# Performance work log

Measured on AMD Instinct MI355X. Metric: run time of the kernel, lower is better.

## Reference

```python
import jax, jax.numpy as jnp
import numpy as np

EPS = 1e-5

def layer_norm(x, g, b):
    mu = jnp.mean(x, axis=-1, keepdims=True)
    var = jnp.mean(jnp.square(x - mu), axis=-1, keepdims=True)
    return (x - mu) * jax.lax.rsqrt(var + EPS) * g + b

def setup_inputs() -> dict:
    key = jax.random.key(0)
    B, N, IN_D, S, D = 64, 4096, 256, 8, 256
    ks = jax.random.split(key, 20)
    scale = lambda fan_in: 1.0 / np.sqrt(fan_in)
    u = lambda k, shape, s: jax.random.uniform(k, shape, jnp.float32, -s, s)
    return {
        "inputs": jax.random.normal(ks[0], (B, N, IN_D), jnp.float32),
        "noise": jax.random.normal(ks[1], (B, S, D), jnp.float32),
        "slots_mu": jax.random.normal(ks[2], (1, S, D), jnp.float32),
        "slots_sigma": jnp.ones((1, S, D), jnp.float32) * 0.1,
        "Wq": u(ks[3], (D, D), scale(D)), "bq": u(ks[4], (D,), scale(D)),
        "Wk": u(ks[5], (D, IN_D), scale(IN_D)), "bk": u(ks[6], (D,), scale(IN_D)),
        "Wv": u(ks[7], (D, IN_D), scale(IN_D)), "bv": u(ks[8], (D,), scale(IN_D)),
        "W_ih": u(ks[9], (3 * D, D), scale(D)), "b_ih": u(ks[10], (3 * D,), scale(D)),
        "W_hh": u(ks[11], (3 * D, D), scale(D)), "b_hh": u(ks[12], (3 * D,), scale(D)),
        "W1": u(ks[13], (D, D), scale(D)), "b1": u(ks[14], (D,), scale(D)),
        "W2": u(ks[15], (D, D), scale(D)), "b2": u(ks[16], (D,), scale(D)),
        "ln_slots_g": jnp.ones((D,), jnp.float32), "ln_slots_b": jnp.zeros((D,), jnp.float32),
        "ln_mlp_g": jnp.ones((D,), jnp.float32), "ln_mlp_b": jnp.zeros((D,), jnp.float32),
    }

def gru_cell(x, h, W_ih, b_ih, W_hh, b_hh):
    # PyTorch GRUCell: gates ordered (reset, update, new)
    gi = x @ W_ih.T + b_ih  # [B*S, 3D]
    gh = h @ W_hh.T + b_hh
    i_r, i_z, i_n = jnp.split(gi, 3, axis=-1)
    h_r, h_z, h_n = jnp.split(gh, 3, axis=-1)
    r = jax.nn.sigmoid(i_r + h_r)
    z = jax.nn.sigmoid(i_z + h_z)
    n = jnp.tanh(i_n + r * h_n)
    return (1.0 - z) * n + z * h

def reference(inputs, noise, slots_mu, slots_sigma, Wq, bq, Wk, bk, Wv, bv,
              W_ih, b_ih, W_hh, b_hh, W1, b1, W2, b2,
              ln_slots_g, ln_slots_b, ln_mlp_g, ln_mlp_b):
    B, N, _ = inputs.shape
    _, S, D = noise.shape
    num_iterations = 3
    slots = slots_mu + slots_sigma * noise  # [B, S, D]
    # k, v are loop-invariant; hoist the big GEMMs out of the iteration loop
    k = jnp.einsum('bnd,ed->bne', inputs, Wk) + bk  # [B, N, D]
    v = jnp.einsum('bnd,ed->bne', inputs, Wv) + bv  # [B, N, D]
    inv_sqrt_d = 1.0 / np.sqrt(D)
    for _ in range(num_iterations):
        slots_prev = slots
        q = layer_norm(slots, ln_slots_g, ln_slots_b) @ Wq.T + bq  # [B, S, D]
        attn_logits = jnp.einsum('bsd,bnd->bsn', q, k) * inv_sqrt_d
        attn = jax.nn.softmax(attn_logits, axis=-1)  # softmax over inputs (dim=-1)
        updates = jnp.einsum('bsn,bnd->bsd', attn, v)  # [B, S, D]
        h_new = gru_cell(updates.reshape(-1, D), slots_prev.reshape(-1, D),
                         W_ih, b_ih, W_hh, b_hh).reshape(B, S, D)
        slots = slots_prev + h_new  # residual around GRU (as in source)
        hidden = jax.nn.relu(layer_norm(slots, ln_mlp_g, ln_mlp_b) @ W1.T + b1)
        slots = slots + (hidden @ W2.T + b2)
    return slots
```

## Files before the change

### kernel.cpp

```cpp
#include <hip/hip_runtime.h>


constexpr int Bn = 64;
constexpr int Nn = 4096;
constexpr int Dd = 256;
constexpr int Ss = 8;
constexpr int CH = 16;
constexpr float EPSF = 1e-5f;

#define DEV __device__ __forceinline__

using short8 = __attribute__((ext_vector_type(8))) short;
using f32x4 = __attribute__((ext_vector_type(4))) float;
union U8 { short8 s; uint4 u; };

DEV unsigned bfpack2(float lo, float hi) {
  unsigned ul = __float_as_uint(lo), uh = __float_as_uint(hi);
  ul = (ul + 0x7FFFu + ((ul >> 16) & 1u)) >> 16;
  uh = (uh + 0x7FFFu + ((uh >> 16) & 1u)) & 0xFFFF0000u;
  return ul | uh;
}
DEV unsigned short bf16r(float x) {
  unsigned u = __float_as_uint(x);
  u = (u + 0x7FFFu + ((u >> 16) & 1u)) >> 16;
  return (unsigned short)u;
}
DEV float rsum32(float v) {
  v += __shfl_xor(v, 1); v += __shfl_xor(v, 2); v += __shfl_xor(v, 4);
  v += __shfl_xor(v, 8); v += __shfl_xor(v, 16);
  return v;
}
DEV float sigm(float x) { return 1.f / (1.f + __expf(-x)); }

template <int NK>
DEV void load_af(short8* a, const unsigned short* base, int lda, int m16, int quad) {
  const unsigned short* p = base + m16 * lda + quad * 8;
#pragma unroll
  for (int kk = 0; kk < NK; ++kk) a[kk] = *(const short8*)(p + kk * 32);
}
template <int NK>
DEV f32x4 gemm_tile(const short8* a, const unsigned short* wr, float binit) {
  f32x4 acc = {binit, binit, binit, binit};
#pragma unroll
  for (int kk = 0; kk < NK; ++kk) {
    short8 b = *(const short8*)(wr + kk * 32);
    acc = __builtin_amdgcn_mfma_f32_16x16x32_bf16(a[kk], b, acc, 0, 0, 0);
  }
  return acc;
}

DEV void ln_row8(const float* x, const float* g, const float* b, int d0,
                 unsigned short* dst) {
  float s = x[0] + x[1] + x[2] + x[3] + x[4] + x[5] + x[6] + x[7];
  float mu = rsum32(s) * (1.f / 256.f);
  float q = 0.f;
#pragma unroll
  for (int j = 0; j < 8; ++j) { float d = x[j] - mu; q += d * d; }
  float rs = rsqrtf(rsum32(q) * (1.f / 256.f) + EPSF);
  float o[8];
#pragma unroll
  for (int j = 0; j < 8; ++j) o[j] = (x[j] - mu) * rs * g[d0 + j] + b[d0 + j];
  uint4 w;
  w.x = bfpack2(o[0], o[1]); w.y = bfpack2(o[2], o[3]);
  w.z = bfpack2(o[4], o[5]); w.w = bfpack2(o[6], o[7]);
  *(uint4*)dst = w;
}

__global__ __launch_bounds__(256) void k_wqk(const float* __restrict__ Wq,
                                             const float* __restrict__ Wk,
                                             const float* __restrict__ bq,
                                             unsigned short* __restrict__ Wqk_b,
                                             float* __restrict__ bqk) {
  int tid = threadIdx.x, c = blockIdx.x;
  if (c < 256) {
    float acc = 0.f;
    for (int e = 0; e < 256; ++e) acc += Wq[e * 256 + tid] * Wk[e * 256 + c];
    Wqk_b[c * 256 + tid] = bf16r(acc);
  } else {
    float acc = 0.f;
    for (int e = 0; e < 256; ++e) acc += bq[e] * Wk[e * 256 + tid];
    bqk[tid] = acc;
  }
}

__global__ __launch_bounds__(256) void k_conv(
    const float* __restrict__ Wv, const float* __restrict__ Wih,
    const float* __restrict__ Whh, const float* __restrict__ W1,
    const float* __restrict__ W2,
    const float* __restrict__ bih, const float* __restrict__ bhh,
    unsigned* Wv_b, unsigned* Wzr_b, unsigned* Win_b, unsigned* Whn_b,
    unsigned* W1_b, unsigned* W2_b, float* bzr) {
  if (blockIdx.x >= 1152) {
    int i = (blockIdx.x - 1152) * 256 + threadIdx.x;
    if (i < 512) bzr[i] = bih[i] + bhh[i];
    return;
  }
  int p = blockIdx.x * 256 + threadIdx.x;
  const float* src; unsigned* dst;
  if (p < 32768) { src = Wv + 2 * p; dst = Wv_b + p; }
  else if (p < 163840) {
    int q = p - 32768, row = q >> 8, col = (q & 255) * 2;
    src = (col < 256) ? (Wih + row * 256 + col) : (Whh + row * 256 + col - 256);
    dst = Wzr_b + q;
  }
  else if (p < 196608) { int q = p - 163840; src = Wih + 512 * 256 + 2 * q; dst = Win_b + q; }
  else if (p < 229376) { int q = p - 196608; src = Whh + 512 * 256 + 2 * q; dst = Whn_b + q; }
  else if (p < 262144) { int q = p - 229376; src = W1 + 2 * q; dst = W1_b + q; }
  else { int q = p - 262144; src = W2 + 2 * q; dst = W2_b + q; }
  dst[0] = bfpack2(src[0], src[1]);
}

__global__ __launch_bounds__(256) void k_xconv(const float* __restrict__ xin,
                                               unsigned* __restrict__ xbf) {
#pragma unroll
  for (int j = 0; j < 4; ++j) {
    int flat = blockIdx.x * 1024 + j * 256 + threadIdx.x;
    const float4* src = (const float4*)(xin + (size_t)flat * 8);
    float4 v0 = src[0], v1 = src[1];
    uint4 o;
    o.x = bfpack2(v0.x, v0.y); o.y = bfpack2(v0.z, v0.w);
    o.z = bfpack2(v1.x, v1.y); o.w = bfpack2(v1.z, v1.w);
    ((uint4*)xbf)[flat] = o;
  }
}

__global__ __launch_bounds__(512) void k_qk0(const float* __restrict__ noise,
                                             const float* __restrict__ s_mu,
                                             const float* __restrict__ s_sg,
                                             const float* __restrict__ gsl,
                                             const float* __restrict__ bsl,
                                             const unsigned short* __restrict__ Wqk_b,
                                             const float* __restrict__ bqk,
                                             float* __restrict__ slots,
                                             float* __restrict__ qk) {
  __shared__ __align__(16) unsigned short lnb[16 * 264];
  const int tid = threadIdx.x, bb = blockIdx.x;
  const int lane = tid & 63, wave = tid >> 6;
  const int m16 = lane & 15, quad = lane >> 4;
  const int row = tid >> 5, l32 = tid & 31, d0 = l32 * 8;
  {
    const int grow = bb * 16 + row;
    const int sidx = (grow & 7) * 256 + d0;
    const float* np = noise + (size_t)grow * 256 + d0;
    float4 n0 = *(const float4*)np, n1 = *(const float4*)(np + 4);
    float4 m0 = *(const float4*)(s_mu + sidx), m1 = *(const float4*)(s_mu + sidx + 4);
    float4 g0 = *(const float4*)(s_sg + sidx), g1 = *(const float4*)(s_sg + sidx + 4);
    float x[8] = {m0.x + g0.x * n0.x, m0.y + g0.y * n0.y,
                  m0.z + g0.z * n0.z, m0.w + g0.w * n0.w,
                  m1.x + g1.x * n1.x, m1.y + g1.y * n1.y,
                  m1.z + g1.z * n1.z, m1.w + g1.w * n1.w};
    float* sp_ = slots + (size_t)grow * 256 + d0;
    float4 o0, o1;
    o0.x = x[0]; o0.y = x[1]; o0.z = x[2]; o0.w = x[3];
    o1.x = x[4]; o1.y = x[5]; o1.z = x[6]; o1.w = x[7];
    *(float4*)sp_ = o0; *(float4*)(sp_ + 4) = o1;
    ln_row8(x, gsl, bsl, d0, lnb + row * 264 + d0);
  }
  __syncthreads();
  short8 a8[8];
  load_af<8>(a8, lnb, 264, m16, quad);
#pragma unroll
  for (int i = 0; i < 2; ++i) {
    int t = wave + 8 * i;
    f32x4 acc = gemm_tile<8>(a8, Wqk_b + (size_t)(t * 16 + m16) * 256 + quad * 8,
                             bqk[t * 16 + m16]);
#pragma unroll
    for (int r = 0; r < 4; ++r)
      qk[(size_t)(bb * 16 + quad * 4 + r) * 256 + t * 16 + m16] = acc[r] * 0.0625f;
  }
}

__global__ __launch_bounds__(256) void k_attn(const unsigned* __restrict__ xbf,
                                              const float* __restrict__ qk,
                                              float* __restrict__ pl,
                                              float* __restrict__ pu) {
  __shared__ __align__(16) unsigned xt[2][128 * 65];
  __shared__ __align__(16) unsigned pp[2][32 * 17];
  __shared__ __align__(16) float lred[4][16];
  const int tid = threadIdx.x;
  const int lane = tid & 63, wave = tid >> 6;
  const int m16 = lane & 15, quad = lane >> 4;
  const int c = blockIdx.x, b = blockIdx.y;
  const int pb = (b * CH + c) * 8;
  const unsigned psel = (m16 & 1) ? 0x07060302u : 0x05040100u;

  short8 aq[8];
  {
    const float* qrow = qk + (size_t)(b * 8 + (m16 & 7)) * 256 + quad * 8;
#pragma unroll
    for (int kk = 0; kk < 8; ++kk) {
      U8 f;
      float4 q0 = *(const float4*)(qrow + kk * 32);
      float4 q1 = *(const float4*)(qrow + kk * 32 + 4);
      f.u.x = bfpack2(q0.x, q0.y); f.u.y = bfpack2(q0.z, q0.w);
      f.u.z = bfpack2(q1.x, q1.y); f.u.w = bfpack2(q1.z, q1.w);
      if (m16 >= 8) { f.u.x = 0u; f.u.y = 0u; f.u.z = 0u; f.u.w = 0u; }
      aq[kk] = f.s;
    }
  }
  float lacc[4] = {0.f, 0.f, 0.f, 0.f};
  f32x4 acc[4];
#pragma unroll
  for (int t = 0; t < 4; ++t) acc[t] = (f32x4){0.f, 0.f, 0.f, 0.f};
  const int d0w = wave * 64;

  const size_t row0 = (size_t)b * Nn + (size_t)c * 256;
  const uint4* xb4 = (const uint4*)xbf;

  uint4 pr[8];
#pragma unroll
  for (int i = 0; i < 8; ++i) {
    int flat = i * 256 + tid, n = flat >> 5, od = flat & 31;
    pr[i] = xb4[(row0 + n) * 32 + od];
  }

  for (int ch = 0; ch < 4; ++ch) {
    const int p = ch & 1;
    unsigned* xtb = xt[p];
#pragma unroll
    for (int i = 0; i < 8; ++i) {
      int flat = i * 256 + tid, n = flat >> 5, od = flat & 31, rb = od * 4;
      xtb[(rb + 0) * 65 + n] = pr[i].x;
      xtb[(rb + 1) * 65 + n] = pr[i].y;
      xtb[(rb + 2) * 65 + n] = pr[i].z;
      xtb[(rb + 3) * 65 + n] = pr[i].w;
    }
    if (ch + 1 < 4) {
      const size_t nb = row0 + (size_t)(ch + 1) * 64;
#pragma unroll
      for (int i = 0; i < 8; ++i) {
        int flat = i * 256 + tid, n = flat >> 5, od = flat & 31;
        pr[i] = xb4[(nb + n) * 32 + od];
      }
    }
    {
      const int nt = wave;
      const size_t arow = row0 + (size_t)ch * 64 + nt * 16 + m16;
      f32x4 pacc = (f32x4){0.f, 0.f, 0.f, 0.f};
#pragma unroll
      for (int kk = 0; kk < 8; ++kk) {
        U8 bf;
        bf.u = xb4[arow * 32 + kk * 4 + quad];
        pacc = __builtin_amdgcn_mfma_f32_16x16x32_bf16(aq[kk], bf.s, pacc, 0, 0, 0);
      }
      const int xrow = nt * 16 + m16;
      unsigned short* pps = (unsigned short*)pp[p];
#pragma unroll
      for (int r = 0; r < 4; ++r) {
        float pv = __expf(pacc[r]);
        lacc[r] += pv;
        pps[((xrow >> 1) * 17 + quad * 4 + r) * 2 + (xrow & 1)] = bf16r(pv);
      }
    }
    __syncthreads();
    const unsigned* ppb = pp[p];
#pragma unroll
    for (int nh = 0; nh < 2; ++nh) {
      U8 bp;
      bp.u.x = ppb[(nh * 16 + quad * 4 + 0) * 17 + m16];
      bp.u.y = ppb[(nh * 16 + quad * 4 + 1) * 17 + m16];
      bp.u.z = ppb[(nh * 16 + quad * 4 + 2) * 17 + m16];
      bp.u.w = ppb[(nh * 16 + quad * 4 + 3) * 17 + m16];
#pragma unroll
      for (int t = 0; t < 4; ++t) {
        int d = d0w + t * 16 + m16;
        const unsigned* xr = xtb + (d >> 1) * 65 + nh * 32 + quad * 8;
        unsigned u0 = xr[0], u1 = xr[1], u2 = xr[2], u3 = xr[3];
        unsigned u4 = xr[4], u5 = xr[5], u6 = xr[6], u7 = xr[7];
        U8 af;
        af.u.x = __builtin_amdgcn_perm(u1, u0, psel);
        af.u.y = __builtin_amdgcn_perm(u3, u2, psel);
        af.u.z = __builtin_amdgcn_perm(u5, u4, psel);
        af.u.w = __builtin_amdgcn_perm(u7, u6, psel);
        acc[t] = __builtin_amdgcn_mfma_f32_16x16x32_bf16(af.s, bp.s, acc[t], 0, 0, 0);
      }
    }
  }
  if (m16 < 8) {
#pragma unroll
    for (int t = 0; t < 4; ++t)
#pragma unroll
      for (int r = 0; r < 4; ++r)
        pu[(size_t)(pb + m16) * 256 + d0w + t * 16 + quad * 4 + r] = acc[t][r];
  }
#pragma unroll
  for (int r = 0; r < 4; ++r) {
    float v = lacc[r];
    v += __shfl_xor(v, 1); v += __shfl_xor(v, 2);
    v += __shfl_xor(v, 4); v += __shfl_xor(v, 8);
    if (m16 == 0) lred[wave][quad * 4 + r] = v;
  }
  __syncthreads();
  if (tid < 8)
    pl[pb + tid] = lred[0][tid] + lred[1][tid] + lred[2][tid] + lred[3][tid];
}

__global__ __launch_bounds__(512) void k_upd(
    const float* __restrict__ pl, const float* __restrict__ pu,
    const unsigned short* __restrict__ Wv_b, const float* __restrict__ bv,
    const unsigned short* __restrict__ Wzr_b, const float* __restrict__ bzr,
    const unsigned short* __restrict__ Win_b, const float* __restrict__ bin,
    const unsigned short* __restrict__ Whn_b, const float* __restrict__ bhn,
    const unsigned short* __restrict__ W1_b, const float* __restrict__ b1,
    const unsigned short* __restrict__ W2_b, const float* __restrict__ b2,
    const float* __restrict__ gml, const float* __restrict__ bml,
    const float* __restrict__ gsl, const float* __restrict__ bsl,
    const unsigned short* __restrict__ Wqk_b, const float* __restrict__ bqk,
    float* __restrict__ slots, float* __restrict__ qk, float* __restrict__ dout) {
  __shared__ __align__(16) unsigned short cat[16 * 520];
  __shared__ __align__(16) float sp[16 * 260];
  __shared__ __align__(16) float s1[16 * 260];
  __shared__ __align__(16) unsigned short lnb[16 * 264];
  const int tid = threadIdx.x, bb = blockIdx.x;
  const int lane = tid & 63, wave = tid >> 6;
  const int m16 = lane & 15, quad = lane >> 4;
  const int row = tid >> 5, l32 = tid & 31, d0 = l32 * 8;
  const int bat = 2 * bb + (row >> 3), sl = row & 7;
  {
    float L = 0.f;
#pragma unroll
    for (int cc = 0; cc < 16; ++cc) L += pl[(bat * 16 + cc) * 8 + sl];
    float li = 1.f / L;
    float a[8] = {0.f, 0.f, 0.f, 0.f, 0.f, 0.f, 0.f, 0.f};
    for (int cc = 0; cc < 16; ++cc) {
      const float* pp_ = pu + ((size_t)(bat * 16 + cc) * 8 + sl) * 256 + d0;
      float4 v0 = *(const float4*)pp_, v1 = *(const float4*)(pp_ + 4);
      a[0] += v0.x; a[1] += v0.y; a[2] += v0.z; a[3] += v0.w;
      a[4] += v1.x; a[5] += v1.y; a[6] += v1.z; a[7] += v1.w;
    }
    uint4 o;
    o.x = bfpack2(a[0] * li, a[1] * li); o.y = bfpack2(a[2] * li, a[3] * li);
    o.z = bfpack2(a[4] * li, a[5] * li); o.w = bfpack2(a[6] * li, a[7] * li);
    *(uint4*)(cat + row * 520 + d0) = o;
    const float* sp_ = slots + (size_t)(bb * 16 + row) * 256 + d0;
    float4 h0 = *(const float4*)sp_, h1 = *(const float4*)(sp_ + 4);
    *(float4*)(sp + row * 260 + d0) = h0;
    *(float4*)(sp + row * 260 + d0 + 4) = h1;
    uint4 hb;
    hb.x = bfpack2(h0.x, h0.y); hb.y = bfpack2(h0.z, h0.w);
    hb.z = bfpack2(h1.x, h1.y); hb.w = bfpack2(h1.z, h1.w);
    *(uint4*)(cat + row * 520 + 256 + d0) = hb;
  }
  __syncthreads();
  short8 afr[16];
  load_af<8>(afr, cat, 520, m16, quad);
  f32x4 accv[2];
#pragma unroll
  for (int i = 0; i < 2; ++i) {
    int t = wave + 8 * i;
    accv[i] = gemm_tile<8>(afr, Wv_b + (size_t)(t * 16 + m16) * 256 + quad * 8,
                           bv[t * 16 + m16]);
  }
  __syncthreads();
#pragma unroll
  for (int i = 0; i < 2; ++i) {
    int t = wave + 8 * i;
#pragma unroll
    for (int r = 0; r < 4; ++r)
      cat[(quad * 4 + r) * 520 + t * 16 + m16] = bf16r(accv[i][r]);
  }
  __syncthreads();
  load_af<16>(afr, cat, 520, m16, quad);
  f32x4 rr[2], zz[2];
#pragma unroll
  for (int i = 0; i < 2; ++i) {
    int t = wave + 8 * i;
    f32x4 ar = gemm_tile<16>(afr, Wzr_b + (size_t)(t * 16 + m16) * 512 + quad * 8,
                             bzr[t * 16 + m16]);
    f32x4 az = gemm_tile<16>(afr, Wzr_b + (size_t)((t + 16) * 16 + m16) * 512 + quad * 8,
                             bzr[(t + 16) * 16 + m16]);
#pragma unroll
    for (int r = 0; r < 4; ++r) { rr[i][r] = sigm(ar[r]); zz[i][r] = sigm(az[r]); }
  }
#pragma unroll
  for (int i = 0; i < 2; ++i) {
    int t = wave + 8 * i, col = t * 16 + m16;
    f32x4 ain = gemm_tile<8>(afr, Win_b + (size_t)(t * 16 + m16) * 256 + quad * 8,
                             bin[col]);
    f32x4 ahn = gemm_tile<8>(afr + 8, Whn_b + (size_t)(t * 16 + m16) * 256 + quad * 8,
                             bhn[col]);
#pragma unroll
    for (int r = 0; r < 4; ++r) {
      int rw = quad * 4 + r;
      float nin = ain[r] + rr[i][r] * ahn[r];
      float nn = 1.f - 2.f / (__expf(2.f * nin) + 1.f);
      float hpc = sp[rw * 260 + col];
      s1[rw * 260 + col] = hpc + (1.f - zz[i][r]) * nn + zz[i][r] * hpc;
    }
  }
  __syncthreads();
  {
    const float* s1r = s1 + row * 260 + d0;
    float4 v0 = *(const float4*)s1r, v1 = *(const float4*)(s1r + 4);
    float x[8] = {v0.x, v0.y, v0.z, v0.w, v1.x, v1.y, v1.z, v1.w};
    ln_row8(x, gml, bml, d0, lnb + row * 264 + d0);
  }
  __syncthreads();
  load_af<8>(afr, lnb, 264, m16, quad);
#pragma unroll
  for (int i = 0; i < 2; ++i) {
    int t = wave + 8 * i;
    f32x4 acc = gemm_tile<8>(afr, W1_b + (size_t)(t * 16 + m16) * 256 + quad * 8,
                             b1[t * 16 + m16]);
#pragma unroll
    for (int r = 0; r < 4; ++r)
      cat[(quad * 4 + r) * 520 + t * 16 + m16] = bf16r(fmaxf(acc[r], 0.f));
  }
  __syncthreads();
  load_af<8>(afr, cat, 520, m16, quad);
#pragma unroll
  for (int i = 0; i < 2; ++i) {
    int t = wave + 8 * i;
    f32x4 acc = gemm_tile<8>(afr, W2_b + (size_t)(t * 16 + m16) * 256 + quad * 8,
                             b2[t * 16 + m16]);
#pragma unroll
    for (int r = 0; r < 4; ++r) {
      int rw = quad * 4 + r, col = t * 16 + m16;
      float v = acc[r] + s1[rw * 260 + col];
      size_t gi = (size_t)(bb * 16 + rw) * 256 + col;
      slots[gi] = v;
      if (dout) dout[gi] = v;
      sp[rw * 260 + col] = v;
    }
  }
  __syncthreads();
  {
    const float* spr = sp + row * 260 + d0;
    float4 v0 = *(const float4*)spr, v1 = *(const float4*)(spr + 4);
    float x[8] = {v0.x, v0.y, v0.z, v0.w, v1.x, v1.y, v1.z, v1.w};
    ln_row8(x, gsl, bsl, d0, lnb + row * 264 + d0);
  }
  __syncthreads();
  load_af<8>(afr, lnb, 264, m16, quad);
#pragma unroll
  for (int i = 0; i < 2; ++i) {
    int t = wave + 8 * i;
    f32x4 acc = gemm_tile<8>(afr, Wqk_b + (size_t)(t * 16 + m16) * 256 + quad * 8,
                             bqk[t * 16 + m16]);
#pragma unroll
    for (int r = 0; r < 4; ++r)
      qk[(size_t)(bb * 16 + quad * 4 + r) * 256 + t * 16 + m16] = acc[r] * 0.0625f;
  }
}

extern "C" void kernel_launch(void* const* d_in, const int* in_sizes, int n_in,
                              void* d_out, int out_size, void* d_ws, size_t ws_size,
                              hipStream_t stream) {
  const float* inputs = (const float*)d_in[0];
  const float* noise = (const float*)d_in[1];
  const float* s_mu = (const float*)d_in[2];
  const float* s_sg = (const float*)d_in[3];
  const float* Wq = (const float*)d_in[4];
  const float* bq = (const float*)d_in[5];
  const float* Wk = (const float*)d_in[6];
  const float* Wv = (const float*)d_in[8];
  const float* bv = (const float*)d_in[9];
  const float* Wih = (const float*)d_in[10];
  const float* bih = (const float*)d_in[11];
  const float* Whh = (const float*)d_in[12];
  const float* bhh = (const float*)d_in[13];
  const float* W1 = (const float*)d_in[14];
  const float* b1 = (const float*)d_in[15];
  const float* W2 = (const float*)d_in[16];
  const float* b2 = (const float*)d_in[17];
  const float* gsl = (const float*)d_in[18];
  const float* bsl = (const float*)d_in[19];
  const float* gml = (const float*)d_in[20];
  const float* bml = (const float*)d_in[21];
  float* out = (float*)d_out;

  char* wsb = (char*)d_ws;
  unsigned* xbf = (unsigned*)wsb;
  float* fp = (float*)(wsb + (size_t)Bn * Nn * Dd * 2);
  float* slots = fp; fp += Bn * Ss * Dd;
  float* qk = fp;    fp += Bn * Ss * Dd;
  float* bqk = fp;   fp += Dd;
  float* pl = fp;    fp += Bn * CH * Ss;
  float* pu = fp;    fp += Bn * CH * Ss * Dd;
  float* bzr = fp;   fp += 512;
  unsigned short* wb = (unsigned short*)fp;
  unsigned short* Wv_b = wb;  wb += 65536;
  unsigned short* Wzr_b = wb; wb += 262144;
  unsigned short* Win_b = wb; wb += 65536;
  unsigned short* Whn_b = wb; wb += 65536;
  unsigned short* W1_b = wb;  wb += 65536;
  unsigned short* W2_b = wb;  wb += 65536;
  unsigned short* Wqk_b = wb; wb += 65536;
  (void)in_sizes; (void)n_in; (void)out_size; (void)ws_size;

  k_xconv<<<dim3(8192), dim3(256), 0, stream>>>(inputs, xbf);
  k_wqk<<<dim3(257), dim3(256), 0, stream>>>(Wq, Wk, bq, Wqk_b, bqk);
  k_conv<<<dim3(1154), dim3(256), 0, stream>>>(
      Wv, Wih, Whh, W1, W2, bih, bhh, (unsigned*)Wv_b, (unsigned*)Wzr_b,
      (unsigned*)Win_b, (unsigned*)Whn_b, (unsigned*)W1_b, (unsigned*)W2_b, bzr);
  k_qk0<<<dim3(32), dim3(512), 0, stream>>>(noise, s_mu, s_sg, gsl, bsl, Wqk_b, bqk,
                                            slots, qk);
  for (int it = 0; it < 3; ++it) {
    k_attn<<<dim3(CH, Bn), dim3(256), 0, stream>>>(xbf, qk, pl, pu);
    k_upd<<<dim3(32), dim3(512), 0, stream>>>(
        pl, pu, Wv_b, bv, Wzr_b, bzr, Win_b, bih + 512, Whn_b, bhh + 512, W1_b, b1,
        W2_b, b2, gml, bml, gsl, bsl, Wqk_b, bqk, slots, qk, (it == 2) ? out : nullptr);
  }
}
```

Baseline: 699.1 us.

## Quantize inputs and attention probs to FP8 and use fp8 MFMA in attention

Converts the pre-converted input tensor from bf16 to FP8 E4M3 via a software quantizer, halving the bytes streamed by each of the three attention passes. The attention kernel now uses fp8 MFMA for both the logits and the probs-times-inputs products, staging row and transposed copies in shared memory instead of reading rows twice from global. The qk scaling moves into the exp, and the weight-prep kernels are merged into one launch with an 8-column register-blocked Wq·Wk product. FP8 rounding of inputs, queries and softmax numerators may lose accuracy against the fp32 reference.

Measured after the change: 678.1 us. -3.0%, faster.

```diff
diff --git a/kernel.cpp b/kernel.cpp
--- a/kernel.cpp
+++ b/kernel.cpp
@@ -13,6 +13,7 @@
 using short8 = __attribute__((ext_vector_type(8))) short;
 using f32x4 = __attribute__((ext_vector_type(4))) float;
 union U8 { short8 s; uint4 u; };
+union LL { unsigned u[2]; long long l; };
 
 DEV unsigned bfpack2(float lo, float hi) {
   unsigned ul = __float_as_uint(lo), uh = __float_as_uint(hi);
@@ -25,6 +26,22 @@
   u = (u + 0x7FFFu + ((u >> 16) & 1u)) >> 16;
   return (unsigned short)u;
 }
+DEV unsigned f8q(float x) {
+  unsigned u = __float_as_uint(x), s = (u >> 24) & 0x80u;
+  float a = __uint_as_float(u & 0x7FFFFFFFu);
+  if (a >= 448.f) return s | 0x7Eu;
+  if (a < 0.015625f) {
+    int m = (int)rintf(a * 512.f);
+    return s | (unsigned)m;
+  }
+  unsigned v = (u & 0x7FFFFFFFu) + 0x7FFFFu + ((u >> 20) & 1u);
+  unsigned E = (v >> 23) - 120u;
+  unsigned M = (v >> 20) & 7u;
+  if (E > 15u) return s | 0x7Eu;
+  unsigned r = (E << 3) | M;
+  if (r > 0x7Eu) r = 0x7Eu;
+  return s | r;
+}
 DEV float rsum32(float v) {
   v += __shfl_xor(v, 1); v += __shfl_xor(v, 2); v += __shfl_xor(v, 4);
   v += __shfl_xor(v, 8); v += __shfl_xor(v, 16);
@@ -66,61 +83,65 @@
   *(uint4*)dst = w;
 }
 
-__global__ __launch_bounds__(256) void k_wqk(const float* __restrict__ Wq,
-                                             const float* __restrict__ Wk,
-                                             const float* __restrict__ bq,
-                                             unsigned short* __restrict__ Wqk_b,
-                                             float* __restrict__ bqk) {
-  int tid = threadIdx.x, c = blockIdx.x;
-  if (c < 256) {
-    float acc = 0.f;
-    for (int e = 0; e < 256; ++e) acc += Wq[e * 256 + tid] * Wk[e * 256 + c];
-    Wqk_b[c * 256 + tid] = bf16r(acc);
-  } else {
+__global__ __launch_bounds__(256) void k_prep(
+    const float* __restrict__ Wq, const float* __restrict__ Wk,
+    const float* __restrict__ bq, unsigned short* __restrict__ Wqk_b,
+    float* __restrict__ bqk, const float* __restrict__ Wv,
+    const float* __restrict__ Wih, const float* __restrict__ Whh,
+    const float* __restrict__ W1, const float* __restrict__ W2,
+    const float* __restrict__ bih, const float* __restrict__ bhh,
+    unsigned* Wv_b, unsigned* Wzr_b, unsigned* Win_b, unsigned* Whn_b,
+    unsigned* W1_b, unsigned* W2_b, float* bzr) {
+  const int u = blockIdx.x, tid = threadIdx.x;
+  if (u < 32) {
+    const int c0 = u * 8;
+    float acc[8] = {0.f, 0.f, 0.f, 0.f, 0.f, 0.f, 0.f, 0.f};
+    for (int e = 0; e < 256; ++e) {
+      float wq = Wq[e * 256 + tid];
+      const float* wk = Wk + e * 256 + c0;
+#pragma unroll
+      for (int j = 0; j < 8; ++j) acc[j] += wq * wk[j];
+    }
+#pragma unroll
+    for (int j = 0; j < 8; ++j) Wqk_b[(c0 + j) * 256 + tid] = bf16r(acc[j]);
+  } else if (u == 32) {
     float acc = 0.f;
     for (int e = 0; e < 256; ++e) acc += bq[e] * Wk[e * 256 + tid];
     bqk[tid] = acc;
-  }
-}
-
-__global__ __launch_bounds__(256) void k_conv(
-    const float* __restrict__ Wv, const float* __restrict__ Wih,
-    const float* __restrict__ Whh, const float* __restrict__ W1,
-    const float* __restrict__ W2,
-    const float* __restrict__ bih, const float* __restrict__ bhh,
-    unsigned* Wv_b, unsigned* Wzr_b, unsigned* Win_b, unsigned* Whn_b,
-    unsigned* W1_b, unsigned* W2_b, float* bzr) {
-  if (blockIdx.x >= 1152) {
-    int i = (blockIdx.x - 1152) * 256 + threadIdx.x;
-    if (i < 512) bzr[i] = bih[i] + bhh[i];
-    return;
-  }
-  int p = blockIdx.x * 256 + threadIdx.x;
-  const float* src; unsigned* dst;
-  if (p < 32768) { src = Wv + 2 * p; dst = Wv_b + p; }
-  else if (p < 163840) {
-    int q = p - 32768, row = q >> 8, col = (q & 255) * 2;
-    src = (col < 256) ? (Wih + row * 256 + col) : (Whh + row * 256 + col - 256);
-    dst = Wzr_b + q;
-  }
-  else if (p < 196608) { int q = p - 163840; src = Wih + 512 * 256 + 2 * q; dst = Win_b + q; }
-  else if (p < 229376) { int q = p - 196608; src = Whh + 512 * 256 + 2 * q; dst = Whn_b + q; }
-  else if (p < 262144) { int q = p - 229376; src = W1 + 2 * q; dst = W1_b + q; }
-  else { int q = p - 262144; src = W2 + 2 * q; dst = W2_b + q; }
-  dst[0] = bfpack2(src[0], src[1]);
+  } else {
+    int cu = u - 33;
+    if (cu >= 1152) {
+      int i = (cu - 1152) * 256 + tid;
+      if (i < 512) bzr[i] = bih[i] + bhh[i];
+      return;
+    }
+    int p = cu * 256 + tid;
+    const float* src; unsigned* dst;
+    if (p < 32768) { src = Wv + 2 * p; dst = Wv_b + p; }
+    else if (p < 163840) {
+      int q = p - 32768, row = q >> 8, col = (q & 255) * 2;
+      src = (col < 256) ? (Wih + row * 256 + col) : (Whh + row * 256 + col - 256);
+      dst = Wzr_b + q;
+    }
+    else if (p < 196608) { int q = p - 163840; src = Wih + 512 * 256 + 2 * q; dst = Win_b + q; }
+    else if (p < 229376) { int q = p - 196608; src = Whh + 512 * 256 + 2 * q; dst = Whn_b + q; }
+    else if (p < 262144) { int q = p - 229376; src = W1 + 2 * q; dst = W1_b + q; }
+    else { int q = p - 262144; src = W2 + 2 * q; dst = W2_b + q; }
+    dst[0] = bfpack2(src[0], src[1]);
+  }
 }
 
 __global__ __launch_bounds__(256) void k_xconv(const float* __restrict__ xin,
-                                               unsigned* __restrict__ xbf) {
+                                               unsigned char* __restrict__ xbf) {
 #pragma unroll
   for (int j = 0; j < 4; ++j) {
     int flat = blockIdx.x * 1024 + j * 256 + threadIdx.x;
     const float4* src = (const float4*)(xin + (size_t)flat * 8);
     float4 v0 = src[0], v1 = src[1];
-    uint4 o;
-    o.x = bfpack2(v0.x, v0.y); o.y = bfpack2(v0.z, v0.w);
-    o.z = bfpack2(v1.x, v1.y); o.w = bfpack2(v1.z, v1.w);
-    ((uint4*)xbf)[flat] = o;
+    uint2 o;
+    o.x = f8q(v0.x) | (f8q(v0.y) << 8) | (f8q(v0.z) << 16) | (f8q(v0.w) << 24);
+    o.y = f8q(v1.x) | (f8q(v1.y) << 8) | (f8q(v1.z) << 16) | (f8q(v1.w) << 24);
+    ((uint2*)xbf)[flat] = o;
   }
 }
 
@@ -166,36 +187,36 @@
                              bqk[t * 16 + m16]);
 #pragma unroll
     for (int r = 0; r < 4; ++r)
-      qk[(size_t)(bb * 16 + quad * 4 + r) * 256 + t * 16 + m16] = acc[r] * 0.0625f;
-  }
-}
-
-__global__ __launch_bounds__(256) void k_attn(const unsigned* __restrict__ xbf,
+      qk[(size_t)(bb * 16 + quad * 4 + r) * 256 + t * 16 + m16] = acc[r];
+  }
+}
+
+__global__ __launch_bounds__(256) void k_attn(const unsigned char* __restrict__ xbf,
                                               const float* __restrict__ qk,
                                               float* __restrict__ pl,
                                               float* __restrict__ pu) {
-  __shared__ __align__(16) unsigned xt[2][128 * 65];
-  __shared__ __align__(16) unsigned pp[2][32 * 17];
+  __shared__ __align__(16) unsigned xr[64 * 68];
+  __shared__ __align__(16) unsigned xt[64 * 68];
+  __shared__ __align__(16) unsigned char pp[16 * 72];
   __shared__ __align__(16) float lred[4][16];
   const int tid = threadIdx.x;
   const int lane = tid & 63, wave = tid >> 6;
   const int m16 = lane & 15, quad = lane >> 4;
   const int c = blockIdx.x, b = blockIdx.y;
   const int pb = (b * CH + c) * 8;
-  const unsigned psel = (m16 & 1) ? 0x07060302u : 0x05040100u;
-
-  short8 aq[8];
+  const size_t row0 = (size_t)b * Nn + (size_t)c * 256;
+
+  LL aq[8];
   {
     const float* qrow = qk + (size_t)(b * 8 + (m16 & 7)) * 256 + quad * 8;
 #pragma unroll
     for (int kk = 0; kk < 8; ++kk) {
-      U8 f;
       float4 q0 = *(const float4*)(qrow + kk * 32);
       float4 q1 = *(const float4*)(qrow + kk * 32 + 4);
-      f.u.x = bfpack2(q0.x, q0.y); f.u.y = bfpack2(q0.z, q0.w);
-      f.u.z = bfpack2(q1.x, q1.y); f.u.w = bfpack2(q1.z, q1.w);
-      if (m16 >= 8) { f.u.x = 0u; f.u.y = 0u; f.u.z = 0u; f.u.w = 0u; }
-      aq[kk] = f.s;
+      unsigned lo = f8q(q0.x) | (f8q(q0.y) << 8) | (f8q(q0.z) << 16) | (f8q(q0.w) << 24);
+      unsigned hi = f8q(q1.x) | (f8q(q1.y) << 8) | (f8q(q1.z) << 16) | (f8q(q1.w) << 24);
+      if (m16 >= 8) { lo = 0u; hi = 0u; }
+      aq[kk].u[0] = lo; aq[kk].u[1] = hi;
     }
   }
   float lacc[4] = {0.f, 0.f, 0.f, 0.f};
@@ -204,77 +225,74 @@
   for (int t = 0; t < 4; ++t) acc[t] = (f32x4){0.f, 0.f, 0.f, 0.f};
   const int d0w = wave * 64;
 
-  const size_t row0 = (size_t)b * Nn + (size_t)c * 256;
   const uint4* xb4 = (const uint4*)xbf;
-
-  uint4 pr[8];
-#pragma unroll
-  for (int i = 0; i < 8; ++i) {
-    int flat = i * 256 + tid, n = flat >> 5, od = flat & 31;
-    pr[i] = xb4[(row0 + n) * 32 + od];
+  uint4 pr[4];
+#pragma unroll
+  for (int i = 0; i < 4; ++i) {
+    int flat = i * 256 + tid, n = flat >> 4, od = flat & 15;
+    pr[i] = xb4[(row0 + n) * 16 + od];
   }
 
   for (int ch = 0; ch < 4; ++ch) {
-    const int p = ch & 1;
-    unsigned* xtb = xt[p];
-#pragma unroll
-    for (int i = 0; i < 8; ++i) {
-      int flat = i * 256 + tid, n = flat >> 5, od = flat & 31, rb = od * 4;
-      xtb[(rb + 0) * 65 + n] = pr[i].x;
-      xtb[(rb + 1) * 65 + n] = pr[i].y;
-      xtb[(rb + 2) * 65 + n] = pr[i].z;
-      xtb[(rb + 3) * 65 + n] = pr[i].w;
-    }
+#pragma unroll
+    for (int i = 0; i < 4; ++i) {
+      int flat = i * 256 + tid, n = flat >> 4, od = flat & 15;
+      *(uint4*)(xr + n * 68 + od * 4) = pr[i];
+      xt[(od * 4 + 0) * 68 + n] = pr[i].x;
+      xt[(od * 4 + 1) * 68 + n] = pr[i].y;
+      xt[(od * 4 + 2) * 68 + n] = pr[i].z;
+      xt[(od * 4 + 3) * 68 + n] = pr[i].w;
+    }
+    __syncthreads();
     if (ch + 1 < 4) {
       const size_t nb = row0 + (size_t)(ch + 1) * 64;
 #pragma unroll
-      for (int i = 0; i < 8; ++i) {
-        int flat = i * 256 + tid, n = flat >> 5, od = flat & 31;
-        pr[i] = xb4[(nb + n) * 32 + od];
+      for (int i = 0; i < 4; ++i) {
+        int flat = i * 256 + tid, n = flat >> 4, od = flat & 15;
+        pr[i] = xb4[(nb + n) * 16 + od];
       }
     }
     {
       const int nt = wave;
-      const size_t arow = row0 + (size_t)ch * 64 + nt * 16 + m16;
       f32x4 pacc = (f32x4){0.f, 0.f, 0.f, 0.f};
+      const unsigned* xrr = xr + (nt * 16 + m16) * 68 + quad * 2;
 #pragma unroll
       for (int kk = 0; kk < 8; ++kk) {
-        U8 bf;
-        bf.u = xb4[arow * 32 + kk * 4 + quad];
-        pacc = __builtin_amdgcn_mfma_f32_16x16x32_bf16(aq[kk], bf.s, pacc, 0, 0, 0);
+        LL bf;
+        bf.l = *(const long long*)(xrr + kk * 8);
+        pacc = __builtin_amdgcn_mfma_f32_16x16x32_fp8_fp8(aq[kk].l, bf.l, pacc, 0, 0, 0);
       }
-      const int xrow = nt * 16 + m16;
-      unsigned short* pps = (unsigned short*)pp[p];
+      const int n = nt * 16 + m16;
 #pragma unroll
       for (int r = 0; r < 4; ++r) {
-        float pv = __expf(pacc[r]);
-        lacc[r] += pv;
-        pps[((xrow >> 1) * 17 + quad * 4 + r) * 2 + (xrow & 1)] = bf16r(pv);
+        float p = __expf(pacc[r] * 0.0625f);
+        lacc[r] += p;
+        pp[(quad * 4 + r) * 72 + n] = (unsigned char)f8q(p);
       }
     }
     __syncthreads();
-    const unsigned* ppb = pp[p];
+    const unsigned bsel = (m16 & 3) | (((m16 & 3) + 4) << 8);
 #pragma unroll
     for (int nh = 0; nh < 2; ++nh) {
-      U8 bp;
-      bp.u.x = ppb[(nh * 16 + quad * 4 + 0) * 17 + m16];
-      bp.u.y = ppb[(nh * 16 + quad * 4 + 1) * 17 + m16];
-      bp.u.z = ppb[(nh * 16 + quad * 4 + 2) * 17 + m16];
-      bp.u.w = ppb[(nh * 16 + quad * 4 + 3) * 17 + m16];
+      LL bp;
+      bp.l = *(const long long*)(pp + m16 * 72 + nh * 32 + quad * 8);
 #pragma unroll
       for (int t = 0; t < 4; ++t) {
-        int d = d0w + t * 16 + m16;
-        const unsigned* xr = xtb + (d >> 1) * 65 + nh * 32 + quad * 8;
-        unsigned u0 = xr[0], u1 = xr[1], u2 = xr[2], u3 = xr[3];
-        unsigned u4 = xr[4], u5 = xr[5], u6 = xr[6], u7 = xr[7];
-        U8 af;
-        af.u.x = __builtin_amdgcn_perm(u1, u0, psel);
-        af.u.y = __builtin_amdgcn_perm(u3, u2, psel);
-        af.u.z = __builtin_amdgcn_perm(u5, u4, psel);
-        af.u.w = __builtin_amdgcn_perm(u7, u6, psel);
-        acc[t] = __builtin_amdgcn_mfma_f32_16x16x32_bf16(af.s, bp.s, acc[t], 0, 0, 0);
+        int dq = (d0w + t * 16 + m16) >> 2;
+        const unsigned* xtp = xt + dq * 68 + nh * 32 + quad * 8;
+        uint4 w0 = *(const uint4*)xtp;
+        uint4 w1 = *(const uint4*)(xtp + 4);
+        unsigned e0 = __builtin_amdgcn_perm(w0.y, w0.x, bsel);
+        unsigned e1 = __builtin_amdgcn_perm(w0.w, w0.z, bsel);
+        unsigned e2 = __builtin_amdgcn_perm(w1.y, w1.x, bsel);
+        unsigned e3 = __builtin_amdgcn_perm(w1.w, w1.z, bsel);
+        LL af;
+        af.u[0] = __builtin_amdgcn_perm(e1, e0, 0x05040100u);
+        af.u[1] = __builtin_amdgcn_perm(e3, e2, 0x05040100u);
+        acc[t] = __builtin_amdgcn_mfma_f32_16x16x32_fp8_fp8(af.l, bp.l, acc[t], 0, 0, 0);
       }
     }
+    __syncthreads();
   }
   if (m16 < 8) {
 #pragma unroll
@@ -439,7 +457,7 @@
                              bqk[t * 16 + m16]);
 #pragma unroll
     for (int r = 0; r < 4; ++r)
-      qk[(size_t)(bb * 16 + quad * 4 + r) * 256 + t * 16 + m16] = acc[r] * 0.0625f;
+      qk[(size_t)(bb * 16 + quad * 4 + r) * 256 + t * 16 + m16] = acc[r];
   }
 }
 
@@ -470,7 +488,7 @@
   float* out = (float*)d_out;
 
   char* wsb = (char*)d_ws;
-  unsigned* xbf = (unsigned*)wsb;
+  unsigned char* xbf = (unsigned char*)wsb;
   float* fp = (float*)(wsb + (size_t)Bn * Nn * Dd * 2);
   float* slots = fp; fp += Bn * Ss * Dd;
   float* qk = fp;    fp += Bn * Ss * Dd;
@@ -489,10 +507,10 @@
   (void)in_sizes; (void)n_in; (void)out_size; (void)ws_size;
 
   k_xconv<<<dim3(8192), dim3(256), 0, stream>>>(inputs, xbf);
-  k_wqk<<<dim3(257), dim3(256), 0, stream>>>(Wq, Wk, bq, Wqk_b, bqk);
-  k_conv<<<dim3(1154), dim3(256), 0, stream>>>(
-      Wv, Wih, Whh, W1, W2, bih, bhh, (unsigned*)Wv_b, (unsigned*)Wzr_b,
-      (unsigned*)Win_b, (unsigned*)Whn_b, (unsigned*)W1_b, (unsigned*)W2_b, bzr);
+  k_prep<<<dim3(1187), dim3(256), 0, stream>>>(
+      Wq, Wk, bq, Wqk_b, bqk, Wv, Wih, Whh, W1, W2, bih, bhh, (unsigned*)Wv_b,
+      (unsigned*)Wzr_b, (unsigned*)Win_b, (unsigned*)Whn_b, (unsigned*)W1_b,
+      (unsigned*)W2_b, bzr);
   k_qk0<<<dim3(32), dim3(512), 0, stream>>>(noise, s_mu, s_sg, gsl, bsl, Wqk_b, bqk,
                                             slots, qk);
   for (int it = 0; it < 3; ++it) {
```
